# Optimization experiments

Measured on AMD Instinct MI355X. Metric: run time of the kernel, lower is better.

The kernel has to match this reference:

```python
import jax, jax.numpy as jnp
import numpy as np

EMBED_DIM = 768
NUM_HEADS = 12
HEAD_DIM = EMBED_DIM // NUM_HEADS


def setup_inputs() -> dict:
    key = jax.random.key(0)
    ks = jax.random.split(key, 9)
    B, S, D = 2, 2048, EMBED_DIM
    scale = 1.0 / np.sqrt(D)
    x = jax.random.normal(ks[0], (B, S, D), dtype=jnp.float32)
    Wq = jax.random.normal(ks[1], (D, D), dtype=jnp.float32) * scale
    bq = jax.random.normal(ks[2], (D,), dtype=jnp.float32) * 0.01
    Wk = jax.random.normal(ks[3], (D, D), dtype=jnp.float32) * scale
    bk = jax.random.normal(ks[4], (D,), dtype=jnp.float32) * 0.01
    Wv = jax.random.normal(ks[5], (D, D), dtype=jnp.float32) * scale
    bv = jax.random.normal(ks[6], (D,), dtype=jnp.float32) * 0.01
    Wo = jax.random.normal(ks[7], (D, D), dtype=jnp.float32) * scale
    bo = jax.random.normal(ks[8], (D,), dtype=jnp.float32) * 0.01
    return {"x": x, "Wq": Wq, "bq": bq, "Wk": Wk, "bk": bk,
            "Wv": Wv, "bv": bv, "Wo": Wo, "bo": bo}


def reference(x, Wq, bq, Wk, bk, Wv, bv, Wo, bo):
    B, S, D = x.shape
    H, Dh = NUM_HEADS, HEAD_DIM
    # separate QKV projections (weights stored [in, out] so y = x @ W + b)
    q = (x @ Wq + bq).reshape(B, S, H, Dh)
    k = (x @ Wk + bk).reshape(B, S, H, Dh)
    v = (x @ Wv + bv).reshape(B, S, H, Dh)
    # NOTE: original module applies NO 1/sqrt(head_dim) scaling
    scores = jnp.einsum('bqhd,bkhd->bhqk', q, k)          # [B,H,S,S] materialized
    attn = jax.nn.softmax(scores, axis=-1)
    ctx = jnp.einsum('bhqk,bkhd->bqhd', attn, v)          # [B,S,H,Dh]
    out = ctx.reshape(B, S, D) @ Wo + bo
    return out
```

## Files before the change

### kernel.cpp

```cpp
#include <hip/hip_runtime.h>
#include <hip/hip_bf16.h>


typedef __attribute__((ext_vector_type(8))) short short8;
typedef __attribute__((ext_vector_type(4))) float float4e;

__device__ __forceinline__ ushort f2bf(float f) {
    union { float f; unsigned u; } v; v.f = f;
    unsigned r = v.u + 0x7FFF + ((v.u >> 16) & 1);
    return (ushort)(r >> 16);
}

__device__ __forceinline__ unsigned pk2bf(float a, float b) {
    float2 t; t.x = a; t.y = b;
    __hip_bfloat162 h = __float22bfloat162_rn(t);
    union { __hip_bfloat162 h; unsigned u; } cv; cv.h = h;
    return cv.u;
}

__device__ __forceinline__ void async_cp16(const ushort* g, ushort* l) {
    __builtin_amdgcn_global_load_lds(
        (const __attribute__((address_space(1))) unsigned int*)g,
        (__attribute__((address_space(3))) unsigned int*)l,
        16, 0, 0);
}

__global__ __launch_bounds__(256) void cast_f32_bf16(
    const float* __restrict__ in, ushort* __restrict__ out, int n4)
{
    int i = blockIdx.x * blockDim.x + threadIdx.x;
    if (i < n4) {
        float4 v = *(const float4*)&in[(size_t)i * 4];
        ushort4 o;
        o.x = f2bf(v.x); o.y = f2bf(v.y); o.z = f2bf(v.z); o.w = f2bf(v.w);
        *(ushort4*)&out[(size_t)i * 4] = o;
    }
}

__global__ __launch_bounds__(256) void transpose_cast_w4(
    const float* __restrict__ W0, const float* __restrict__ W1,
    const float* __restrict__ W2, const float* __restrict__ W3,
    ushort* __restrict__ WtBase)
{
    __shared__ float t[64][65];
    const int z = blockIdx.z;
    const float* W = (z == 0) ? W0 : (z == 1) ? W1 : (z == 2) ? W2 : W3;
    ushort* Wt = WtBase + (size_t)z * (768u * 768u);

    const int tid = threadIdx.x;
    const int c  = tid & 63;
    const int rg = tid >> 6;
    const int k0 = blockIdx.y * 64, n0 = blockIdx.x * 64;
    #pragma unroll
    for (int r = 0; r < 16; ++r) {
        const int row = rg * 16 + r;
        t[row][c] = W[(size_t)(k0 + row) * 768 + n0 + c];
    }
    __syncthreads();
    #pragma unroll
    for (int r = 0; r < 16; ++r) {
        const int row = rg * 16 + r;
        Wt[(size_t)(n0 + row) * 768 + k0 + c] = f2bf(t[c][row]);
    }
}

__global__ __launch_bounds__(256) void transpose_v(
    const ushort* __restrict__ Vb, ushort* __restrict__ VT)
{
    __shared__ ushort t[64][72];
    const int tid = threadIdx.x;
    const int b = blockIdx.z, h = blockIdx.y, s0 = blockIdx.x * 64;
    const int lr = tid >> 3;
    const int lc = (tid & 7) * 8;

    #pragma unroll
    for (int half = 0; half < 64; half += 32) {
        const int row = lr + half;
        *(uint4*)&t[row][lc] =
            *(const uint4*)&Vb[(size_t)(b * 2048 + s0 + row) * 768 + h * 64 + lc];
    }
    __syncthreads();
    #pragma unroll
    for (int half = 0; half < 64; half += 32) {
        const int d = lr + half;
        ushort tmp[8];
        #pragma unroll
        for (int i = 0; i < 8; ++i) tmp[i] = t[lc + i][d];
        *(uint4*)&VT[((size_t)(b * 12 + h) * 64 + d) * 2048 + s0 + lc] =
            *(const uint4*)tmp;
    }
}

__global__ __launch_bounds__(256) void gemm_qkv_fused(
    const ushort* __restrict__ A, const ushort* __restrict__ Bt,
    const float* __restrict__ bq, const float* __restrict__ bk,
    const float* __restrict__ bv, ushort* __restrict__ Outbase)
{
    constexpr int K = 768;
    __shared__ ushort As[128][32];
    __shared__ ushort Bs[128][32];

    const int tid  = threadIdx.x;
    const int w    = tid >> 6;
    const int lane = tid & 63;
    const int l16  = lane & 15;
    const int quad = lane >> 4;
    const int wr   = (w >> 1) * 64;
    const int wc   = (w & 1) * 64;
    const int row0 = blockIdx.y * 128, col0 = blockIdx.x * 128;

    const int r4 = lane >> 2;
    const int c8 = (lane & 3) * 8;

    float4e acc[4][4];
    #pragma unroll
    for (int mi = 0; mi < 4; ++mi)
        #pragma unroll
        for (int ni = 0; ni < 4; ++ni) acc[mi][ni] = (float4e){0.f,0.f,0.f,0.f};

    for (int k0 = 0; k0 < K; k0 += 32) {
        #pragma unroll
        for (int i = 0; i < 2; ++i) {
            const int rr = w * 32 + i * 16;
            async_cp16(&A [(size_t)(row0 + rr + r4) * K + k0 + c8], &As[rr][0]);
            async_cp16(&Bt[(size_t)(col0 + rr + r4) * K + k0 + c8], &Bs[rr][0]);
        }
        __syncthreads();

        short8 af[4], bf[4];
        #pragma unroll
        for (int i = 0; i < 4; ++i) {
            af[i] = *(const short8*)&As[wr + i * 16 + l16][quad * 8];
            bf[i] = *(const short8*)&Bs[wc + i * 16 + l16][quad * 8];
        }
        #pragma unroll
        for (int mi = 0; mi < 4; ++mi)
            #pragma unroll
            for (int ni = 0; ni < 4; ++ni)
                acc[mi][ni] = __builtin_amdgcn_mfma_f32_16x16x32_bf16(
                    af[mi], bf[ni], acc[mi][ni], 0, 0, 0);
        __syncthreads();
    }

    const int seg = (col0 >= 1536) ? 2 : (col0 >= 768 ? 1 : 0);
    const float* bias = (seg == 0) ? bq : (seg == 1) ? bk : bv;
    const int ncol0 = col0 - seg * 768 + wc;
    ushort* outp = Outbase + (size_t)seg * (4096u * 768u);

    #pragma unroll
    for (int ni = 0; ni < 4; ++ni) {
        const int col = ncol0 + ni * 16 + l16;
        const float bs = bias[col];
        #pragma unroll
        for (int mi = 0; mi < 4; ++mi) {
            #pragma unroll
            for (int r = 0; r < 4; ++r) {
                const int row = row0 + wr + mi * 16 + quad * 4 + r;
                outp[(size_t)row * 768 + col] = f2bf(acc[mi][ni][r] + bs);
            }
        }
    }
}

__global__ __launch_bounds__(256) void gemm_wo_128(
    const ushort* __restrict__ A, const ushort* __restrict__ Bt,
    const float* __restrict__ bias, float* __restrict__ Cout)
{
    constexpr int K = 768, N = 768;
    __shared__ ushort As[128][40];
    __shared__ ushort Bs[128][40];

    const int tid  = threadIdx.x;
    const int w    = tid >> 6;
    const int lane = tid & 63;
    const int l16  = lane & 15;
    const int quad = lane >> 4;
    const int wr   = (w >> 1) * 64;
    const int wc   = (w & 1) * 64;
    const int row0 = blockIdx.y * 128, col0 = blockIdx.x * 128;
    const int sr = tid >> 2, sc = (tid & 3) * 8;

    float4e acc[4][4];
    #pragma unroll
    for (int mi = 0; mi < 4; ++mi)
        #pragma unroll
        for (int ni = 0; ni < 4; ++ni) acc[mi][ni] = (float4e){0.f,0.f,0.f,0.f};

    uint4 a0 = *(const uint4*)&A [(size_t)(row0 + sr     ) * K + sc];
    uint4 a1 = *(const uint4*)&A [(size_t)(row0 + sr + 64) * K + sc];
    uint4 b0 = *(const uint4*)&Bt[(size_t)(col0 + sr     ) * K + sc];
    uint4 b1 = *(const uint4*)&Bt[(size_t)(col0 + sr + 64) * K + sc];

    for (int k0 = 0; k0 < K; k0 += 32) {
        *(uint4*)&As[sr     ][sc] = a0;
        *(uint4*)&As[sr + 64][sc] = a1;
        *(uint4*)&Bs[sr     ][sc] = b0;
        *(uint4*)&Bs[sr + 64][sc] = b1;
        __syncthreads();

        if (k0 + 32 < K) {
            const int kn = k0 + 32;
            a0 = *(const uint4*)&A [(size_t)(row0 + sr     ) * K + kn + sc];
            a1 = *(const uint4*)&A [(size_t)(row0 + sr + 64) * K + kn + sc];
            b0 = *(const uint4*)&Bt[(size_t)(col0 + sr     ) * K + kn + sc];
            b1 = *(const uint4*)&Bt[(size_t)(col0 + sr + 64) * K + kn + sc];
        }

        short8 af[4], bf[4];
        #pragma unroll
        for (int i = 0; i < 4; ++i) {
            af[i] = *(const short8*)&As[wr + i * 16 + l16][quad * 8];
            bf[i] = *(const short8*)&Bs[wc + i * 16 + l16][quad * 8];
        }
        #pragma unroll
        for (int mi = 0; mi < 4; ++mi)
            #pragma unroll
            for (int ni = 0; ni < 4; ++ni)
                acc[mi][ni] = __builtin_amdgcn_mfma_f32_16x16x32_bf16(
                    af[mi], bf[ni], acc[mi][ni], 0, 0, 0);
        __syncthreads();
    }

    #pragma unroll
    for (int ni = 0; ni < 4; ++ni) {
        const int col = col0 + wc + ni * 16 + l16;
        const float bs = bias[col];
        #pragma unroll
        for (int mi = 0; mi < 4; ++mi) {
            #pragma unroll
            for (int r = 0; r < 4; ++r) {
                const int row = row0 + wr + mi * 16 + quad * 4 + r;
                Cout[(size_t)row * N + col] = acc[mi][ni][r] + bs;
            }
        }
    }
}

__global__ __launch_bounds__(512) void attn_mfma(
    const ushort* __restrict__ Qg, const ushort* __restrict__ Kgl,
    const ushort* __restrict__ VT, ushort* __restrict__ Ctx)
{
    constexpr int S = 2048, D = 768;
    __shared__ ushort Ks [64][72];
    __shared__ ushort Vts[64][72];
    __shared__ ushort Ps [64][72];
    __shared__ float  Osc[4][16][68];
    __shared__ float  Msc[4][16], Lsc[4][16];

    const int tid  = threadIdx.x;
    const int w    = tid >> 6;
    const int wq   = w & 3;
    const int koff = (w >> 2) * 32;
    const int lane = tid & 63;
    const int l16  = lane & 15;
    const int quad = lane >> 4;
    const int b = blockIdx.z, h = blockIdx.y, q0 = blockIdx.x * 64;
    const size_t hc = (size_t)h * 64;

    const size_t qoff = (size_t)(b * S + q0 + wq * 16 + l16) * D + hc + quad * 8;
    const short8 yq0 = *(const short8*)&Qg[qoff];
    const short8 yq1 = *(const short8*)&Qg[qoff + 32];

    float m_ = -1e30f, l_ = 0.f;
    float4e oa[4];
    #pragma unroll
    for (int n = 0; n < 4; ++n) oa[n] = (float4e){0.f, 0.f, 0.f, 0.f};

    const int sr = tid >> 3;
    const int sc = (tid & 7) * 8;
    const size_t vtb = ((size_t)(b * 12 + h) * 64 + sr) * 2048;

    uint4 kf = *(const uint4*)&Kgl[(size_t)(b * S + sr) * D + hc + sc];
    uint4 vf = *(const uint4*)&VT[vtb + sc];

    for (int k0 = 0; k0 < S; k0 += 64) {
        *(uint4*)&Ks [sr][sc] = kf;
        *(uint4*)&Vts[sr][sc] = vf;
        __syncthreads();

        if (k0 + 64 < S) {
            kf = *(const uint4*)&Kgl[(size_t)(b * S + k0 + 64 + sr) * D + hc + sc];
            vf = *(const uint4*)&VT[vtb + k0 + 64 + sc];
        }

        float4e sa[2];
        #pragma unroll
        for (int kb = 0; kb < 2; ++kb) {
            const short8 xk0 = *(const short8*)&Ks[koff + kb * 16 + l16][quad * 8];
            const short8 xk1 = *(const short8*)&Ks[koff + kb * 16 + l16][32 + quad * 8];
            float4e z = (float4e){0.f, 0.f, 0.f, 0.f};
            z      = __builtin_amdgcn_mfma_f32_16x16x32_bf16(xk0, yq0, z, 0, 0, 0);
            sa[kb] = __builtin_amdgcn_mfma_f32_16x16x32_bf16(xk1, yq1, z, 0, 0, 0);
        }

        float mx = -1e30f;
        #pragma unroll
        for (int kb = 0; kb < 2; ++kb)
            #pragma unroll
            for (int r = 0; r < 4; ++r) mx = fmaxf(mx, sa[kb][r]);
        mx = fmaxf(mx, __shfl_xor(mx, 16, 64));
        mx = fmaxf(mx, __shfl_xor(mx, 32, 64));
        const float mn = fmaxf(m_, mx);
        const float alpha = __expf(m_ - mn);
        float p[2][4], ps = 0.f;
        #pragma unroll
        for (int kb = 0; kb < 2; ++kb)
            #pragma unroll
            for (int r = 0; r < 4; ++r) {
                p[kb][r] = __expf(sa[kb][r] - mn);
                ps += p[kb][r];
            }
        ps += __shfl_xor(ps, 16, 64);
        ps += __shfl_xor(ps, 32, 64);
        l_ = l_ * alpha + ps;
        m_ = mn;

        #pragma unroll
        for (int kb = 0; kb < 2; ++kb) {
            uint2 pk;
            pk.x = pk2bf(p[kb][0], p[kb][1]);
            pk.y = pk2bf(p[kb][2], p[kb][3]);
            *(uint2*)&Ps[wq * 16 + l16][koff + kb * 16 + quad * 4] = pk;
        }

        #pragma unroll
        for (int n = 0; n < 4; ++n)
            #pragma unroll
            for (int r = 0; r < 4; ++r) oa[n][r] *= alpha;

        const short8 yp = *(const short8*)&Ps[wq * 16 + l16][koff + quad * 8];
        #pragma unroll
        for (int db = 0; db < 4; ++db) {
            const short8 xv = *(const short8*)&Vts[db * 16 + l16][koff + quad * 8];
            oa[db] = __builtin_amdgcn_mfma_f32_16x16x32_bf16(xv, yp, oa[db], 0, 0, 0);
        }
        __syncthreads();
    }

    if (w >= 4) {
        if (quad == 0) { Msc[wq][l16] = m_; Lsc[wq][l16] = l_; }
        #pragma unroll
        for (int db = 0; db < 4; ++db)
            *(float4*)&Osc[wq][l16][db * 16 + quad * 4] =
                *(const float4*)&oa[db];
    }
    __syncthreads();
    if (w < 4) {
        const float m1 = Msc[wq][l16], l1 = Lsc[wq][l16];
        const float mm = fmaxf(m_, m1);
        const float a0 = __expf(m_ - mm), a1 = __expf(m1 - mm);
        const float inv = 1.0f / (l_ * a0 + l1 * a1);
        const size_t crow = (size_t)(b * S + q0 + wq * 16 + l16) * D + hc;
        #pragma unroll
        for (int db = 0; db < 4; ++db) {
            const float4 o1 = *(const float4*)&Osc[wq][l16][db * 16 + quad * 4];
            uint2 ov;
            ov.x = pk2bf((oa[db][0] * a0 + o1.x * a1) * inv,
                         (oa[db][1] * a0 + o1.y * a1) * inv);
            ov.y = pk2bf((oa[db][2] * a0 + o1.z * a1) * inv,
                         (oa[db][3] * a0 + o1.w * a1) * inv);
            *(uint2*)&Ctx[crow + db * 16 + quad * 4] = ov;
        }
    }
}

extern "C" void kernel_launch(void* const* d_in, const int* in_sizes, int n_in,
                              void* d_out, int out_size, void* d_ws, size_t ws_size,
                              hipStream_t stream)
{
    const float* x  = (const float*)d_in[0];
    const float* Wq = (const float*)d_in[1];
    const float* bq = (const float*)d_in[2];
    const float* Wk = (const float*)d_in[3];
    const float* bk = (const float*)d_in[4];
    const float* Wv = (const float*)d_in[5];
    const float* bv = (const float*)d_in[6];
    const float* Wo = (const float*)d_in[7];
    const float* bo = (const float*)d_in[8];

    const int M = 4096, D = 768;
    const size_t XE = (size_t)M * D;
    const size_t WE = (size_t)D * D;

    ushort* xb   = (ushort*)d_ws;
    ushort* wtq  = xb   + XE;
    ushort* wto  = wtq  + 3 * WE;
    ushort* qb   = wto  + WE;
    ushort* kb   = qb   + XE;
    ushort* vb   = kb   + XE;
    ushort* ctxb = vb   + XE;
    ushort* vt   = xb;

    cast_f32_bf16<<<(int)(XE / 4 / 256), 256, 0, stream>>>(x, xb, (int)(XE / 4));

    transpose_cast_w4<<<dim3(12, 12, 4), 256, 0, stream>>>(Wq, Wk, Wv, Wo, wtq);

    gemm_qkv_fused<<<dim3(2304 / 128, 4096 / 128), 256, 0, stream>>>(
        xb, wtq, bq, bk, bv, qb);

    transpose_v<<<dim3(32, 12, 2), 256, 0, stream>>>(vb, vt);

    attn_mfma<<<dim3(2048 / 64, 12, 2), 512, 0, stream>>>(qb, kb, vt, ctxb);

    gemm_wo_128<<<dim3(768 / 128, 4096 / 128), 256, 0, stream>>>(
        ctxb, wto, bo, (float*)d_out);
}
```

Measured before the change: 191.4 us.

## Double-buffer attention K/V via async global-to-LDS loads with XOR swizzle and lazy rescale

The attention kernel now streams K and V tiles straight into double-buffered, XOR-swizzled LDS using global_load_lds, replacing the register-staged single buffer. This removes one barrier per iteration and overlaps the next tile's load with compute. It also skips the running-max rescale of the accumulator unless the max grows by more than a threshold, and raises wave priority around the MFMA blocks. The unpadded swizzled layout is meant to avoid LDS bank conflicts. The risks are the LDS ordering of async writes relative to the single remaining barrier, and exp overflow headroom from the deferred rescale.

```diff
diff --git a/kernel.cpp b/kernel.cpp
--- a/kernel.cpp
+++ b/kernel.cpp
@@ -241,11 +241,17 @@
     const ushort* __restrict__ VT, ushort* __restrict__ Ctx)
 {
     constexpr int S = 2048, D = 768;
-    __shared__ ushort Ks [64][72];
-    __shared__ ushort Vts[64][72];
-    __shared__ ushort Ps [64][72];
-    __shared__ float  Osc[4][16][68];
-    __shared__ float  Msc[4][16], Lsc[4][16];
+    __shared__ union {
+        struct {
+            ushort Ks [2][64][64];
+            ushort Vts[2][64][64];
+        } s;
+        struct {
+            float Osc[4][16][68];
+            float Msc[4][16], Lsc[4][16];
+        } c;
+    } U;
+    __shared__ ushort Ps[64][64];
 
     const int tid  = threadIdx.x;
     const int w    = tid >> 6;
@@ -261,37 +267,59 @@
     const short8 yq0 = *(const short8*)&Qg[qoff];
     const short8 yq1 = *(const short8*)&Qg[qoff + 32];
 
+    const int sr  = tid >> 3;
+    const int cbg = (tid & 7) ^ (sr & 7);
+    const ushort* srcK = &Kgl[(size_t)(b * S + sr) * D + hc + cbg * 8];
+    const ushort* srcV = &VT[((size_t)(b * 12 + h) * 64 + sr) * 2048 + cbg * 8];
+    ushort* dstK0 = &U.s.Ks [0][w * 8][0];
+    ushort* dstK1 = &U.s.Ks [1][w * 8][0];
+    ushort* dstV0 = &U.s.Vts[0][w * 8][0];
+    ushort* dstV1 = &U.s.Vts[1][w * 8][0];
+
+    int oxk[2][2];
+    #pragma unroll
+    for (int kb = 0; kb < 2; ++kb) {
+        const int krow = koff + kb * 16 + l16;
+        oxk[kb][0] = krow * 64 + (( quad     ) ^ (krow & 7)) * 8;
+        oxk[kb][1] = krow * 64 + (((quad | 4)) ^ (krow & 7)) * 8;
+    }
+    const int oxv0 = l16 * 64 + ((((koff >> 3) + quad)) ^ (l16 & 7)) * 8;
+    const int prow = wq * 16 + l16;
+    const int pxor = (prow & 7) * 2;
+    const int opw0 = prow * 64 + ((((koff >> 2)     + quad)) ^ pxor) * 4;
+    const int opw1 = prow * 64 + ((((koff >> 2) + 4 + quad)) ^ pxor) * 4;
+    const int opr  = prow * 64 + ((((koff >> 2) + quad * 2)) ^ pxor) * 4;
+
     float m_ = -1e30f, l_ = 0.f;
     float4e oa[4];
     #pragma unroll
     for (int n = 0; n < 4; ++n) oa[n] = (float4e){0.f, 0.f, 0.f, 0.f};
 
-    const int sr = tid >> 3;
-    const int sc = (tid & 7) * 8;
-    const size_t vtb = ((size_t)(b * 12 + h) * 64 + sr) * 2048;
-
-    uint4 kf = *(const uint4*)&Kgl[(size_t)(b * S + sr) * D + hc + sc];
-    uint4 vf = *(const uint4*)&VT[vtb + sc];
-
+    async_cp16(srcK, dstK0);
+    async_cp16(srcV, dstV0);
+    __syncthreads();
+
+    #pragma unroll 2
     for (int k0 = 0; k0 < S; k0 += 64) {
-        *(uint4*)&Ks [sr][sc] = kf;
-        *(uint4*)&Vts[sr][sc] = vf;
-        __syncthreads();
-
+        const int cur = (k0 >> 6) & 1;
         if (k0 + 64 < S) {
-            kf = *(const uint4*)&Kgl[(size_t)(b * S + k0 + 64 + sr) * D + hc + sc];
-            vf = *(const uint4*)&VT[vtb + k0 + 64 + sc];
-        }
+            async_cp16(srcK + (size_t)(k0 + 64) * D, cur ? dstK0 : dstK1);
+            async_cp16(srcV + (k0 + 64),             cur ? dstV0 : dstV1);
+        }
+        const ushort* ksb = cur ? &U.s.Ks [1][0][0] : &U.s.Ks [0][0][0];
+        const ushort* vsb = cur ? &U.s.Vts[1][0][0] : &U.s.Vts[0][0][0];
 
         float4e sa[2];
+        __builtin_amdgcn_s_setprio(1);
         #pragma unroll
         for (int kb = 0; kb < 2; ++kb) {
-            const short8 xk0 = *(const short8*)&Ks[koff + kb * 16 + l16][quad * 8];
-            const short8 xk1 = *(const short8*)&Ks[koff + kb * 16 + l16][32 + quad * 8];
+            const short8 xk0 = *(const short8*)&ksb[oxk[kb][0]];
+            const short8 xk1 = *(const short8*)&ksb[oxk[kb][1]];
             float4e z = (float4e){0.f, 0.f, 0.f, 0.f};
             z      = __builtin_amdgcn_mfma_f32_16x16x32_bf16(xk0, yq0, z, 0, 0, 0);
             sa[kb] = __builtin_amdgcn_mfma_f32_16x16x32_bf16(xk1, yq1, z, 0, 0, 0);
         }
+        __builtin_amdgcn_s_setprio(0);
 
         float mx = -1e30f;
         #pragma unroll
@@ -300,60 +328,75 @@
             for (int r = 0; r < 4; ++r) mx = fmaxf(mx, sa[kb][r]);
         mx = fmaxf(mx, __shfl_xor(mx, 16, 64));
         mx = fmaxf(mx, __shfl_xor(mx, 32, 64));
-        const float mn = fmaxf(m_, mx);
-        const float alpha = __expf(m_ - mn);
+
+        const bool full = !__all(mx - m_ <= 8.f);
+        float alpha = 0.f;
+        if (full) {
+            const float mn = fmaxf(m_, mx);
+            alpha = __expf(m_ - mn);
+            l_ *= alpha;
+            m_ = mn;
+        }
+
         float p[2][4], ps = 0.f;
         #pragma unroll
         for (int kb = 0; kb < 2; ++kb)
             #pragma unroll
             for (int r = 0; r < 4; ++r) {
-                p[kb][r] = __expf(sa[kb][r] - mn);
+                p[kb][r] = __expf(sa[kb][r] - m_);
                 ps += p[kb][r];
             }
+
+        {
+            uint2 pk;
+            pk.x = pk2bf(p[0][0], p[0][1]);
+            pk.y = pk2bf(p[0][2], p[0][3]);
+            *(uint2*)&Ps[0][opw0] = pk;
+            pk.x = pk2bf(p[1][0], p[1][1]);
+            pk.y = pk2bf(p[1][2], p[1][3]);
+            *(uint2*)&Ps[0][opw1] = pk;
+        }
+
         ps += __shfl_xor(ps, 16, 64);
         ps += __shfl_xor(ps, 32, 64);
-        l_ = l_ * alpha + ps;
-        m_ = mn;
-
-        #pragma unroll
-        for (int kb = 0; kb < 2; ++kb) {
-            uint2 pk;
-            pk.x = pk2bf(p[kb][0], p[kb][1]);
-            pk.y = pk2bf(p[kb][2], p[kb][3]);
-            *(uint2*)&Ps[wq * 16 + l16][koff + kb * 16 + quad * 4] = pk;
-        }
-
-        #pragma unroll
-        for (int n = 0; n < 4; ++n)
-            #pragma unroll
-            for (int r = 0; r < 4; ++r) oa[n][r] *= alpha;
-
-        const short8 yp = *(const short8*)&Ps[wq * 16 + l16][koff + quad * 8];
+        l_ += ps;
+
+        if (full) {
+            #pragma unroll
+            for (int n = 0; n < 4; ++n)
+                #pragma unroll
+                for (int r = 0; r < 4; ++r) oa[n][r] *= alpha;
+        }
+
+        const short8 yp = *(const short8*)&Ps[0][opr];
+        __builtin_amdgcn_s_setprio(1);
         #pragma unroll
         for (int db = 0; db < 4; ++db) {
-            const short8 xv = *(const short8*)&Vts[db * 16 + l16][koff + quad * 8];
+            const short8 xv = *(const short8*)&vsb[oxv0 + db * 1024];
             oa[db] = __builtin_amdgcn_mfma_f32_16x16x32_bf16(xv, yp, oa[db], 0, 0, 0);
         }
+        __builtin_amdgcn_s_setprio(0);
+
         __syncthreads();
     }
 
     if (w >= 4) {
-        if (quad == 0) { Msc[wq][l16] = m_; Lsc[wq][l16] = l_; }
+        if (quad == 0) { U.c.Msc[wq][l16] = m_; U.c.Lsc[wq][l16] = l_; }
         #pragma unroll
         for (int db = 0; db < 4; ++db)
-            *(float4*)&Osc[wq][l16][db * 16 + quad * 4] =
+            *(float4*)&U.c.Osc[wq][l16][db * 16 + quad * 4] =
                 *(const float4*)&oa[db];
     }
     __syncthreads();
     if (w < 4) {
-        const float m1 = Msc[wq][l16], l1 = Lsc[wq][l16];
+        const float m1 = U.c.Msc[wq][l16], l1 = U.c.Lsc[wq][l16];
         const float mm = fmaxf(m_, m1);
         const float a0 = __expf(m_ - mm), a1 = __expf(m1 - mm);
         const float inv = 1.0f / (l_ * a0 + l1 * a1);
         const size_t crow = (size_t)(b * S + q0 + wq * 16 + l16) * D + hc;
         #pragma unroll
         for (int db = 0; db < 4; ++db) {
-            const float4 o1 = *(const float4*)&Osc[wq][l16][db * 16 + quad * 4];
+            const float4 o1 = *(const float4*)&U.c.Osc[wq][l16][db * 16 + quad * 4];
             uint2 ov;
             ov.x = pk2bf((oa[db][0] * a0 + o1.x * a1) * inv,
                          (oa[db][1] * a0 + o1.y * a1) * inv);
```

New measurement: 187.0 us. -2.3%, faster.
